# Kernel tuning notes

Hardware: AMD Instinct MI355X
Metric: run time of the kernel (lower is better)

Reference implementation:

```python
import jax, jax.numpy as jnp
import numpy as np


def _conv1x1(x, w, b):
    # x: [B,Cin,H,W], w: [Cout,Cin], b: [Cout]
    return jnp.einsum('bchw,oc->bohw', x, w) + b[None, :, None, None]


def setup_inputs() -> dict:
    key = jax.random.key(0)
    ks = jax.random.split(key, 9)
    C, Cb = 256, 128
    B, H, W = 8, 32, 32
    s_in = 1.0 / np.sqrt(C)
    s_bn = 1.0 / np.sqrt(Cb)
    return {
        'x': jax.random.normal(ks[0], (B, C, H, W), dtype=jnp.float32),
        'theta_w': jax.random.uniform(ks[1], (Cb, C), jnp.float32, -s_in, s_in),
        'theta_b': jax.random.uniform(ks[2], (Cb,), jnp.float32, -s_in, s_in),
        'phi_w': jax.random.uniform(ks[3], (Cb, C), jnp.float32, -s_in, s_in),
        'phi_b': jax.random.uniform(ks[4], (Cb,), jnp.float32, -s_in, s_in),
        'g_w': jax.random.uniform(ks[5], (Cb, C), jnp.float32, -s_in, s_in),
        'g_b': jax.random.uniform(ks[6], (Cb,), jnp.float32, -s_in, s_in),
        'W_w': jax.random.uniform(ks[7], (C, Cb), jnp.float32, -s_bn, s_bn),
        'W_b': jax.random.uniform(ks[8], (C,), jnp.float32, -s_bn, s_bn),
    }


def reference(x, theta_w, theta_b, phi_w, phi_b, g_w, g_b, W_w, W_b):
    B, C, H, Wd = x.shape
    Cb = theta_w.shape[0]
    theta = _conv1x1(x, theta_w, theta_b).reshape(-1, Cb)      # [N, Cb] (row-major, as torch)
    phi = _conv1x1(x, phi_w, phi_b).reshape(Cb, -1)            # [Cb, N]
    g = _conv1x1(x, g_w, g_b).reshape(-1, Cb)                  # [N, Cb]
    attn = jax.nn.softmax(theta @ phi, axis=1)                 # [N, N] global attention
    out = (attn @ g).reshape(B, -1, H, Wd)                     # [B, Cb, H, W]
    return _conv1x1(out, W_w, W_b) + x
```

## Files before the change

kernel.cpp:

```cpp
#include <hip/hip_runtime.h>

typedef unsigned short u16;
typedef __attribute__((ext_vector_type(8))) short short8;
typedef __attribute__((ext_vector_type(4))) float f32x4;

__device__ __forceinline__ u16 f2bf(float f){
  union { float f; unsigned u; } v; v.f = f;
  unsigned u = v.u;
  u += 0x7fffu + ((u >> 16) & 1u);
  return (u16)(u >> 16);
}
__device__ __forceinline__ float bf2f(u16 h){
  union { unsigned u; float f; } v; v.u = ((unsigned)h) << 16;
  return v.f;
}

__global__ __launch_bounds__(256) void xcast_kernel(
    const float* __restrict__ x, u16* __restrict__ XT)
{
  __shared__ float tile[64][69];
  const int b = blockIdx.z, c0 = blockIdx.y*64, hw0 = blockIdx.x*64;
  const int t = threadIdx.x;
  {
    int r = t >> 2, cs = (t & 3) * 16;
    const float* s = x + (size_t)(b*256 + c0 + r)*1024 + hw0 + cs;
    #pragma unroll
    for (int i=0;i<4;i++)
      *(float4*)&tile[r][cs + i*4] = *(const float4*)(s + i*4);
  }
  __syncthreads();
  {
    int hr = t >> 2, cc = (t & 3) * 16;
    __align__(16) u16 tmp[16];
    #pragma unroll
    for (int i=0;i<16;i++) tmp[i] = f2bf(tile[cc + i][hr]);
    u16* d = XT + (size_t)(b*1024 + hw0 + hr)*256 + c0 + cc;
    *(uint4*)d     = *(uint4*)&tmp[0];
    *(uint4*)(d+8) = *(uint4*)&tmp[8];
  }
}

__global__ __launch_bounds__(256, 2) void proj_mfma_kernel(
    const u16* __restrict__ XT,
    const float* __restrict__ tw, const float* __restrict__ pw,
    const float* __restrict__ gw,
    const float* __restrict__ tb, const float* __restrict__ pb,
    const float* __restrict__ gb,
    u16* __restrict__ T, u16* __restrict__ PHI, u16* __restrict__ G)
{
  __shared__ __align__(16) u16 Ws[128][136];
  __shared__ __align__(16) u16 Xs[128][136];
  const int proj = blockIdx.x, qg = blockIdx.y;
  const int b = qg >> 3, hw0 = (qg & 7) * 128;
  const int q0 = qg * 128;
  const float* Wf   = (proj==0) ? tw : (proj==1) ? pw : gw;
  const float* bias = (proj==0) ? tb : (proj==1) ? pb : gb;
  u16* out          = (proj==0) ? T  : (proj==1) ? PHI : G;
  const float scale = (proj==0) ? 1.4426950408889634f : 1.0f;
  const int t = threadIdx.x;
  const int wave = t >> 6, lane = t & 63;
  const int quad = lane >> 4, n16 = lane & 15;

  f32x4 acc[8][2];
  #pragma unroll
  for (int mt=0;mt<8;mt++)
    #pragma unroll
    for (int nt=0;nt<2;nt++){ f32x4 z = {0.f,0.f,0.f,0.f}; acc[mt][nt] = z; }

  for (int c0 = 0; c0 < 256; c0 += 128){
    __syncthreads();
    {
      int row = t >> 1, cb = (t & 1) * 64;
      const float* s1 = Wf + (size_t)row*256 + c0 + cb;
      #pragma unroll
      for (int i=0;i<16;i++){
        float4 v = *(const float4*)(s1 + i*4);
        u16* d = &Ws[row][cb + i*4];
        d[0]=f2bf(v.x); d[1]=f2bf(v.y); d[2]=f2bf(v.z); d[3]=f2bf(v.w);
      }
      const u16* s2 = XT + (size_t)(q0 + row)*256 + c0 + cb;
      #pragma unroll
      for (int i=0;i<8;i++)
        *(uint4*)&Xs[row][cb + i*8] = *(const uint4*)(s2 + i*8);
    }
    __syncthreads();
    #pragma unroll
    for (int kc=0; kc<4; kc++){
      short8 xf[2];
      #pragma unroll
      for (int nt=0;nt<2;nt++)
        xf[nt] = *(const short8*)&Xs[wave*32 + nt*16 + n16][kc*32 + quad*8];
      #pragma unroll
      for (int mt=0;mt<8;mt++){
        short8 wf = *(const short8*)&Ws[mt*16 + n16][kc*32 + quad*8];
        #pragma unroll
        for (int nt=0;nt<2;nt++)
          acc[mt][nt] = __builtin_amdgcn_mfma_f32_16x16x32_bf16(wf, xf[nt], acc[mt][nt], 0, 0, 0);
      }
    }
  }
  #pragma unroll
  for (int mt=0;mt<8;mt++){
    float4 bv = *(const float4*)&bias[mt*16 + quad*4];
    float bb[4] = {bv.x, bv.y, bv.z, bv.w};
    #pragma unroll
    for (int nt=0;nt<2;nt++)
      #pragma unroll
      for (int r=0;r<4;r++)
        out[(size_t)b*131072 + (size_t)(mt*16 + quad*4 + r)*1024
            + hw0 + wave*32 + nt*16 + n16] = f2bf((acc[mt][nt][r] + bb[r]) * scale);
  }
}

__global__ __launch_bounds__(256) void transpose_bf_kernel(
    const u16* __restrict__ src, u16* __restrict__ dst, int R, int C)
{
  __shared__ u16 tile[64][72];
  const int t = threadIdx.x;
  const int c0 = blockIdx.x*64, r0 = blockIdx.y*64;
  {
    int rr = t >> 2, cs = (t & 3) * 16;
    const u16* s = src + (size_t)(r0+rr)*C + c0 + cs;
    uint4 a0 = *(const uint4*)s;
    uint4 a1 = *(const uint4*)(s+8);
    *(uint4*)&tile[rr][cs]   = a0;
    *(uint4*)&tile[rr][cs+8] = a1;
  }
  __syncthreads();
  {
    int cc = t >> 2, rs = (t & 3) * 16;
    __align__(16) u16 tmp[16];
    #pragma unroll
    for (int i=0;i<16;i++) tmp[i] = tile[rs+i][cc];
    u16* d = dst + (size_t)(c0+cc)*R + r0 + rs;
    *(uint4*)d     = *(uint4*)&tmp[0];
    *(uint4*)(d+8) = *(uint4*)&tmp[8];
  }
}

__global__ __launch_bounds__(256, 2) void attn_kernel(
    const u16* __restrict__ Tq, const u16* __restrict__ Kk,
    const u16* __restrict__ Vt, u16* __restrict__ Opart,
    float* __restrict__ lpart)
{
  __shared__ __align__(16) u16 Ks[64][136];
  __shared__ __align__(16) u16 Vs[128][72];
  __shared__ __align__(16) u16 Pall[4][4608];

  const int t = threadIdx.x;
  const int wave = t >> 6, lane = t & 63;
  const int quad = lane >> 4, n16 = lane & 15;
  const int s  = blockIdx.x & 15;
  const int qg = blockIdx.x >> 4;
  const int q0 = qg*256 + wave*64;
  u16* Pw = Pall[wave];
  u16*   Os = Opart + (size_t)s * 1048576;
  float* ls = lpart + (size_t)s * 8192;

  short8 qa[4][4];
  #pragma unroll
  for (int mt=0;mt<4;mt++)
    #pragma unroll
    for (int kc=0;kc<4;kc++)
      qa[mt][kc] = *(const short8*)(Tq + (size_t)(q0 + mt*16 + n16)*128 + kc*32 + quad*8);

  f32x4 o[4][8];
  float lp[4];
  #pragma unroll
  for (int mt=0;mt<4;mt++){
    #pragma unroll
    for (int dt=0;dt<8;dt++){ f32x4 z = {0.f,0.f,0.f,0.f}; o[mt][dt] = z; }
    lp[mt] = 0.f;
  }

  const int krow = t >> 2, kcs = (t & 3) * 32;
  const int vrow = t >> 1, vcs = (t & 1) * 32;
  const int wmask = n16 & 14;

  for (int kt = s*8; kt < s*8 + 8; kt++){
    const int key0 = kt * 64;
    __syncthreads();
    #pragma unroll
    for (int i=0;i<4;i++)
      *(uint4*)&Ks[krow][kcs + i*8] =
        *(const uint4*)(Kk + (size_t)(key0 + krow)*128 + kcs + i*8);
    #pragma unroll
    for (int i=0;i<4;i++)
      *(uint4*)&Vs[vrow][vcs + i*8] =
        *(const uint4*)(Vt + (size_t)vrow*8192 + key0 + vcs + i*8);
    __syncthreads();

    #pragma unroll
    for (int ntk=0; ntk<4; ntk++){
      short8 kf[4];
      #pragma unroll
      for (int kc=0;kc<4;kc++)
        kf[kc] = *(const short8*)&Ks[ntk*16 + n16][kc*32 + quad*8];
      #pragma unroll
      for (int mtq=0;mtq<4;mtq++){
        f32x4 sa = {0.f,0.f,0.f,0.f};
        #pragma unroll
        for (int kc=0;kc<4;kc++)
          sa = __builtin_amdgcn_mfma_f32_16x16x32_bf16(kf[kc], qa[mtq][kc], sa, 0, 0, 0);
        u16 pb[4];
        #pragma unroll
        for (int r=0;r<4;r++){
          float pe = __builtin_amdgcn_exp2f(sa[r]);
          lp[mtq] += pe;
          pb[r] = f2bf(pe);
        }
        uint2 pk;
        pk.x = ((unsigned)pb[1] << 16) | pb[0];
        pk.y = ((unsigned)pb[3] << 16) | pb[2];
        *(uint2*)(Pw + (mtq*16 + n16)*72 + (((ntk*4 + quad) ^ wmask) << 2)) = pk;
      }
    }

    __builtin_amdgcn_s_waitcnt(0xC07F);

    #pragma unroll
    for (int kb=0; kb<2; kb++){
      short8 pf[4];
      #pragma unroll
      for (int mtq=0;mtq<4;mtq++)
        pf[mtq] = *(const short8*)(Pw + (mtq*16 + n16)*72 + (((kb*8 + quad*2) ^ wmask) << 2));
      __builtin_amdgcn_s_setprio(1);
      #pragma unroll
      for (int dt=0; dt<8; dt++){
        short8 vfd = *(const short8*)&Vs[dt*16 + n16][kb*32 + quad*8];
        #pragma unroll
        for (int mtq=0;mtq<4;mtq++)
          o[mtq][dt] = __builtin_amdgcn_mfma_f32_16x16x32_bf16(pf[mtq], vfd, o[mtq][dt], 0, 0, 0);
      }
      __builtin_amdgcn_s_setprio(0);
    }
  }

  float l[4];
  #pragma unroll
  for (int mt=0;mt<4;mt++){
    float v = lp[mt];
    v += __shfl_xor(v, 16, 64);
    v += __shfl_xor(v, 32, 64);
    l[mt] = v;
  }

  #pragma unroll
  for (int mt=0;mt<4;mt++){
    #pragma unroll
    for (int r=0;r<4;r++){
      __align__(16) u16 tmp[8];
      #pragma unroll
      for (int dt=0;dt<8;dt++) tmp[dt] = f2bf(o[mt][dt][r]);
      *(uint4*)(Os + (size_t)(q0 + mt*16 + quad*4 + r)*128 + n16*8) = *(uint4*)tmp;
    }
    if (lane < 16)
      ls[q0 + mt*16 + lane] = l[mt];
  }
}

__global__ __launch_bounds__(256) void merge_o_kernel(
    const u16* __restrict__ Opart, const float* __restrict__ lpart, int S,
    u16* __restrict__ OmT)
{
  __shared__ u16 Tm[32][136];
  __shared__ float lrow[32];
  const int t = threadIdx.x;
  const int row0 = blockIdx.x * 32;
  const int b  = row0 >> 10;
  const int j0 = (row0 >> 3) & 127;

  if (t < 32){
    float v = 0.f;
    for (int sp=0; sp<S; sp++) v += lpart[sp*8192 + row0 + t];
    lrow[t] = 1.0f / v;
  }

  const int rl = t >> 3;
  const int cb = (t & 7) * 16;
  float acc[16];
  #pragma unroll
  for (int j=0;j<16;j++) acc[j] = 0.f;
  for (int sp=0; sp<S; sp++){
    const u16* p = Opart + (size_t)sp*1048576 + (size_t)(row0 + rl)*128 + cb;
    #pragma unroll
    for (int q=0;q<2;q++){
      ushort4 v = *(const ushort4*)(p + q*8);
      ushort4 w = *(const ushort4*)(p + q*8 + 4);
      acc[q*8+0] += bf2f(v.x); acc[q*8+1] += bf2f(v.y);
      acc[q*8+2] += bf2f(v.z); acc[q*8+3] += bf2f(v.w);
      acc[q*8+4] += bf2f(w.x); acc[q*8+5] += bf2f(w.y);
      acc[q*8+6] += bf2f(w.z); acc[q*8+7] += bf2f(w.w);
    }
  }
  __syncthreads();
  const float inv = lrow[rl];
  #pragma unroll
  for (int j=0;j<16;j++){
    int cp = cb + j;
    int ch = (cp & 7)*16 + (cp >> 3);
    Tm[rl][ch] = f2bf(acc[j] * inv);
  }
  __syncthreads();
  {
    const int hwhi = t >> 5;
    const int chb  = (t & 31) * 4;
    #pragma unroll
    for (int c=0;c<4;c++){
      int ch = chb + c;
      __align__(8) u16 tmp[4];
      #pragma unroll
      for (int jl=0;jl<4;jl++) tmp[jl] = Tm[jl*8 + hwhi][ch];
      *(uint2*)(OmT + (size_t)(b*1024 + hwhi*128 + ch)*128 + j0) = *(uint2*)tmp;
    }
  }
}

__global__ __launch_bounds__(256, 2) void final_mfma_kernel(
    const float* __restrict__ Ww, const float* __restrict__ Wb,
    const u16* __restrict__ OmT, const float* __restrict__ x,
    float* __restrict__ outp)
{
  __shared__ __align__(16) u16 Ws[64][136];
  __shared__ __align__(16) u16 Os[128][136];
  const int co0 = blockIdx.x * 64, qg = blockIdx.y;
  const int b = qg >> 3, hw0 = (qg & 7) * 128;
  const int q0 = qg * 128;
  const int t = threadIdx.x;
  const int wave = t >> 6, lane = t & 63;
  const int quad = lane >> 4, n16 = lane & 15;

  {
    int row = t >> 2, cbf = (t & 3) * 32;
    const float* sw = Ww + (size_t)(co0 + row)*128 + cbf;
    #pragma unroll
    for (int i=0;i<8;i++){
      float4 v = *(const float4*)(sw + i*4);
      u16* d = &Ws[row][cbf + i*4];
      d[0]=f2bf(v.x); d[1]=f2bf(v.y); d[2]=f2bf(v.z); d[3]=f2bf(v.w);
    }
  }
  {
    int row = t >> 1, cb = (t & 1) * 64;
    const u16* so = OmT + (size_t)(q0 + row)*128 + cb;
    #pragma unroll
    for (int i=0;i<8;i++)
      *(uint4*)&Os[row][cb + i*8] = *(const uint4*)(so + i*8);
  }
  __syncthreads();

  f32x4 acc[4][2];
  #pragma unroll
  for (int mt=0;mt<4;mt++)
    #pragma unroll
    for (int nt=0;nt<2;nt++){ f32x4 z = {0.f,0.f,0.f,0.f}; acc[mt][nt] = z; }

  #pragma unroll
  for (int kc=0; kc<4; kc++){
    short8 xf[2];
    #pragma unroll
    for (int nt=0;nt<2;nt++)
      xf[nt] = *(const short8*)&Os[wave*32 + nt*16 + n16][kc*32 + quad*8];
    #pragma unroll
    for (int mt=0;mt<4;mt++){
      short8 wf = *(const short8*)&Ws[mt*16 + n16][kc*32 + quad*8];
      #pragma unroll
      for (int nt=0;nt<2;nt++)
        acc[mt][nt] = __builtin_amdgcn_mfma_f32_16x16x32_bf16(wf, xf[nt], acc[mt][nt], 0, 0, 0);
    }
  }

  #pragma unroll
  for (int mt=0;mt<4;mt++){
    float4 bv = *(const float4*)&Wb[co0 + mt*16 + quad*4];
    float bb[4] = {bv.x, bv.y, bv.z, bv.w};
    #pragma unroll
    for (int nt=0;nt<2;nt++)
      #pragma unroll
      for (int r=0;r<4;r++){
        size_t idx = (size_t)b*262144 + (size_t)(co0 + mt*16 + quad*4 + r)*1024
                   + hw0 + wave*32 + nt*16 + n16;
        outp[idx] = acc[mt][nt][r] + bb[r] + x[idx];
      }
  }
}

extern "C" void kernel_launch(void* const* d_in, const int* in_sizes, int n_in,
                              void* d_out, int out_size, void* d_ws, size_t ws_size,
                              hipStream_t stream)
{
  (void)in_sizes; (void)n_in; (void)out_size; (void)ws_size;
  const float* x  = (const float*)d_in[0];
  const float* tw = (const float*)d_in[1];
  const float* tb = (const float*)d_in[2];
  const float* pw = (const float*)d_in[3];
  const float* pb = (const float*)d_in[4];
  const float* gw = (const float*)d_in[5];
  const float* gb = (const float*)d_in[6];
  const float* Ww = (const float*)d_in[7];
  const float* Wb = (const float*)d_in[8];
  float* outp = (float*)d_out;

  char* ws = (char*)d_ws;
  const size_t MB = 1u << 20;
  u16*   Tbf   = (u16*)(ws);
  u16*   PHIbf = (u16*)(ws + 2*MB);
  u16*   Gbf   = (u16*)(ws + 4*MB);
  u16*   Kbf   = (u16*)(ws + 6*MB);
  u16*   VTbf  = (u16*)(ws + 8*MB);
  u16*   Opart = (u16*)(ws + 10*MB);
  u16*   XT    = (u16*)(ws + 10*MB);
  float* lpart = (float*)(ws + 2*MB);
  u16*   OmT   = (u16*)(ws + 4*MB);

  xcast_kernel<<<dim3(16, 4, 8), 256, 0, stream>>>(x, XT);
  proj_mfma_kernel<<<dim3(3, 64), 256, 0, stream>>>(XT, tw, pw, gw, tb, pb, gb,
                                                    Tbf, PHIbf, Gbf);
  transpose_bf_kernel<<<dim3(128, 2), 256, 0, stream>>>(PHIbf, Kbf, 128, 8192);
  transpose_bf_kernel<<<dim3(2, 128), 256, 0, stream>>>(Gbf, VTbf, 8192, 128);
  attn_kernel<<<dim3(512), 256, 0, stream>>>(Tbf, Kbf, VTbf, Opart, lpart);
  merge_o_kernel<<<dim3(256), 256, 0, stream>>>(Opart, lpart, 16, OmT);
  final_mfma_kernel<<<dim3(4, 64), 256, 0, stream>>>(Ww, Wb, OmT, x, outp);
}
```

Baseline: 162.9 us.

## Double-buffer K/V tiles via direct global-to-LDS loads in attention kernel

Restructures the attention kernel to use 512-thread blocks (8 waves, 512 queries per block) and double-buffered K/V shared tiles filled with global_load_lds, so the next key tile loads while the current one is computed. The LDS layout drops row padding in favour of an XOR swizzle to avoid bank conflicts. The goal is to hide global-load latency and halve the number of K/V loads per query. In exchange it uses more LDS, allows only one block per CU, and adds a full vmcnt wait plus a barrier every iteration.

```diff
diff --git a/kernel.cpp b/kernel.cpp
--- a/kernel.cpp
+++ b/kernel.cpp
@@ -13,6 +13,11 @@
 __device__ __forceinline__ float bf2f(u16 h){
   union { unsigned u; float f; } v; v.u = ((unsigned)h) << 16;
   return v.f;
+}
+__device__ __forceinline__ void gload16(const u16* g, u16* l){
+  __builtin_amdgcn_global_load_lds(
+      (const __attribute__((address_space(1))) unsigned int*)g,
+      (__attribute__((address_space(3))) unsigned int*)l, 16, 0, 0);
 }
 
 __global__ __launch_bounds__(256) void xcast_kernel(
@@ -138,21 +143,21 @@
   }
 }
 
-__global__ __launch_bounds__(256, 2) void attn_kernel(
+__global__ __launch_bounds__(512, 1) void attn_kernel(
     const u16* __restrict__ Tq, const u16* __restrict__ Kk,
     const u16* __restrict__ Vt, u16* __restrict__ Opart,
     float* __restrict__ lpart)
 {
-  __shared__ __align__(16) u16 Ks[64][136];
-  __shared__ __align__(16) u16 Vs[128][72];
-  __shared__ __align__(16) u16 Pall[4][4608];
+  __shared__ __align__(16) u16 Ks[2][8192];
+  __shared__ __align__(16) u16 Vs[2][8192];
+  __shared__ __align__(16) u16 Pall[8][4096];
 
   const int t = threadIdx.x;
   const int wave = t >> 6, lane = t & 63;
   const int quad = lane >> 4, n16 = lane & 15;
   const int s  = blockIdx.x & 15;
   const int qg = blockIdx.x >> 4;
-  const int q0 = qg*256 + wave*64;
+  const int q0 = qg*512 + wave*64;
   u16* Pw = Pall[wave];
   u16*   Os = Opart + (size_t)s * 1048576;
   float* ls = lpart + (size_t)s * 8192;
@@ -173,29 +178,46 @@
     lp[mt] = 0.f;
   }
 
-  const int krow = t >> 2, kcs = (t & 3) * 32;
-  const int vrow = t >> 1, vcs = (t & 1) * 32;
+  const int ck0   = wave * 2;
+  const int rk_l  = lane >> 4;
+  const int rv_l  = lane >> 3;
+  const int cbk_l = (lane & 15) * 16;
+  const int cbv_l = (lane & 7) * 16;
   const int wmask = n16 & 14;
-
-  for (int kt = s*8; kt < s*8 + 8; kt++){
-    const int key0 = kt * 64;
-    __syncthreads();
-    #pragma unroll
-    for (int i=0;i<4;i++)
-      *(uint4*)&Ks[krow][kcs + i*8] =
-        *(const uint4*)(Kk + (size_t)(key0 + krow)*128 + kcs + i*8);
-    #pragma unroll
-    for (int i=0;i<4;i++)
-      *(uint4*)&Vs[vrow][vcs + i*8] =
-        *(const uint4*)(Vt + (size_t)vrow*8192 + key0 + vcs + i*8);
-    __syncthreads();
+  const int swz   = (n16 & 7) << 4;
+
+  auto STAGE = [&](int bi, int key0){
+    #pragma unroll
+    for (int i=0;i<2;i++){
+      const int ck = ck0 + i;
+      const int rk = ck*4 + rk_l;
+      gload16(Kk + (size_t)(key0 + rk)*128 + ((cbk_l ^ ((rk & 7) << 4)) >> 1),
+              &Ks[bi][ck*512]);
+    }
+    #pragma unroll
+    for (int i=0;i<2;i++){
+      const int ck = ck0 + i;
+      const int rv = ck*8 + rv_l;
+      gload16(Vt + (size_t)rv*8192 + key0 + ((cbv_l ^ ((rv & 7) << 4)) >> 1),
+              &Vs[bi][ck*512]);
+    }
+  };
+
+  STAGE(0, s*512);
+  asm volatile("s_waitcnt vmcnt(0)" ::: "memory");
+  __syncthreads();
+
+  int bi = 0;
+  for (int kt = 0; kt < 8; kt++){
+    if (kt < 7) STAGE(bi^1, (s*8 + kt + 1)*64);
 
     #pragma unroll
     for (int ntk=0; ntk<4; ntk++){
       short8 kf[4];
       #pragma unroll
       for (int kc=0;kc<4;kc++)
-        kf[kc] = *(const short8*)&Ks[ntk*16 + n16][kc*32 + quad*8];
+        kf[kc] = *(const short8*)((const char*)&Ks[bi][0]
+                   + ((ntk*16 + n16) << 8) + ((kc*64 + quad*16) ^ swz));
       #pragma unroll
       for (int mtq=0;mtq<4;mtq++){
         f32x4 sa = {0.f,0.f,0.f,0.f};
@@ -212,7 +234,7 @@
         uint2 pk;
         pk.x = ((unsigned)pb[1] << 16) | pb[0];
         pk.y = ((unsigned)pb[3] << 16) | pb[2];
-        *(uint2*)(Pw + (mtq*16 + n16)*72 + (((ntk*4 + quad) ^ wmask) << 2)) = pk;
+        *(uint2*)(Pw + (mtq*16 + n16)*64 + (((ntk*4 + quad) ^ wmask) << 2)) = pk;
       }
     }
 
@@ -223,16 +245,23 @@
       short8 pf[4];
       #pragma unroll
       for (int mtq=0;mtq<4;mtq++)
-        pf[mtq] = *(const short8*)(Pw + (mtq*16 + n16)*72 + (((kb*8 + quad*2) ^ wmask) << 2));
+        pf[mtq] = *(const short8*)(Pw + (mtq*16 + n16)*64 + (((kb*8 + quad*2) ^ wmask) << 2));
       __builtin_amdgcn_s_setprio(1);
       #pragma unroll
       for (int dt=0; dt<8; dt++){
-        short8 vfd = *(const short8*)&Vs[dt*16 + n16][kb*32 + quad*8];
+        short8 vfd = *(const short8*)((const char*)&Vs[bi][0]
+                       + ((dt*16 + n16) << 7) + ((kb*64 + quad*16) ^ swz));
         #pragma unroll
         for (int mtq=0;mtq<4;mtq++)
           o[mtq][dt] = __builtin_amdgcn_mfma_f32_16x16x32_bf16(pf[mtq], vfd, o[mtq][dt], 0, 0, 0);
       }
       __builtin_amdgcn_s_setprio(0);
+    }
+
+    if (kt < 7){
+      asm volatile("s_waitcnt vmcnt(0)" ::: "memory");
+      __syncthreads();
+      bi ^= 1;
     }
   }
 
@@ -418,7 +447,7 @@
                                                     Tbf, PHIbf, Gbf);
   transpose_bf_kernel<<<dim3(128, 2), 256, 0, stream>>>(PHIbf, Kbf, 128, 8192);
   transpose_bf_kernel<<<dim3(2, 128), 256, 0, stream>>>(Gbf, VTbf, 8192, 128);
-  attn_kernel<<<dim3(512), 256, 0, stream>>>(Tbf, Kbf, VTbf, Opart, lpart);
+  attn_kernel<<<dim3(256), 512, 0, stream>>>(Tbf, Kbf, VTbf, Opart, lpart);
   merge_o_kernel<<<dim3(256), 256, 0, stream>>>(Opart, lpart, 16, OmT);
   final_mfma_kernel<<<dim3(4, 64), 256, 0, stream>>>(Ww, Wb, OmT, x, outp);
 }
```

Result: slower. 223.6 us (+37.2%).

## Split attention block into producer and consumer waves with register-prefetched K/V tiles

Applied to the files above, without the earlier changes.

The attention kernel now launches 512 threads per block. The upper four waves act as producers: they prefetch the next K and V tile into registers while the lower four waves run the QK^T, exp and PV MFMA work on the current tile. The goal is to hide global-load latency behind compute instead of making the compute waves do their own loads between barriers. The cost is doubled block size, with register limits set by launch_bounds(512,2) that may cause spills in the consumers holding large accumulators, and producer waves that sit idle during compute.

```diff
diff --git a/kernel.cpp b/kernel.cpp
--- a/kernel.cpp
+++ b/kernel.cpp
@@ -138,7 +138,7 @@
   }
 }
 
-__global__ __launch_bounds__(256, 2) void attn_kernel(
+__global__ __launch_bounds__(512, 2) void attn_kernel(
     const u16* __restrict__ Tq, const u16* __restrict__ Kk,
     const u16* __restrict__ Vt, u16* __restrict__ Opart,
     float* __restrict__ lpart)
@@ -150,112 +150,135 @@
   const int t = threadIdx.x;
   const int wave = t >> 6, lane = t & 63;
   const int quad = lane >> 4, n16 = lane & 15;
+  const bool producer = (t >= 256);
   const int s  = blockIdx.x & 15;
   const int qg = blockIdx.x >> 4;
-  const int q0 = qg*256 + wave*64;
-  u16* Pw = Pall[wave];
+  const int q0 = qg*256 + (wave & 3)*64;
+  u16* Pw = Pall[wave & 3];
   u16*   Os = Opart + (size_t)s * 1048576;
   float* ls = lpart + (size_t)s * 8192;
 
+  const int pt   = t & 255;
+  const int krow = pt >> 2, kcs = (pt & 3) * 32;
+  const int vrow = pt >> 1, vcs = (pt & 1) * 32;
+  const int wmask = n16 & 14;
+
   short8 qa[4][4];
-  #pragma unroll
-  for (int mt=0;mt<4;mt++)
-    #pragma unroll
-    for (int kc=0;kc<4;kc++)
-      qa[mt][kc] = *(const short8*)(Tq + (size_t)(q0 + mt*16 + n16)*128 + kc*32 + quad*8);
-
   f32x4 o[4][8];
   float lp[4];
-  #pragma unroll
-  for (int mt=0;mt<4;mt++){
-    #pragma unroll
-    for (int dt=0;dt<8;dt++){ f32x4 z = {0.f,0.f,0.f,0.f}; o[mt][dt] = z; }
-    lp[mt] = 0.f;
-  }
-
-  const int krow = t >> 2, kcs = (t & 3) * 32;
-  const int vrow = t >> 1, vcs = (t & 1) * 32;
-  const int wmask = n16 & 14;
-
-  for (int kt = s*8; kt < s*8 + 8; kt++){
-    const int key0 = kt * 64;
+  uint4 kr[4], vr[4];
+
+  if (producer){
+    const int key0 = s*512;
+    #pragma unroll
+    for (int i=0;i<4;i++)
+      kr[i] = *(const uint4*)(Kk + (size_t)(key0 + krow)*128 + kcs + i*8);
+    #pragma unroll
+    for (int i=0;i<4;i++)
+      vr[i] = *(const uint4*)(Vt + (size_t)vrow*8192 + key0 + vcs + i*8);
+  } else {
+    #pragma unroll
+    for (int mt=0;mt<4;mt++)
+      #pragma unroll
+      for (int kc=0;kc<4;kc++)
+        qa[mt][kc] = *(const short8*)(Tq + (size_t)(q0 + mt*16 + n16)*128 + kc*32 + quad*8);
+    #pragma unroll
+    for (int mt=0;mt<4;mt++){
+      #pragma unroll
+      for (int dt=0;dt<8;dt++){ f32x4 z = {0.f,0.f,0.f,0.f}; o[mt][dt] = z; }
+      lp[mt] = 0.f;
+    }
+  }
+
+  for (int kt = 0; kt < 8; kt++){
     __syncthreads();
-    #pragma unroll
-    for (int i=0;i<4;i++)
-      *(uint4*)&Ks[krow][kcs + i*8] =
-        *(const uint4*)(Kk + (size_t)(key0 + krow)*128 + kcs + i*8);
-    #pragma unroll
-    for (int i=0;i<4;i++)
-      *(uint4*)&Vs[vrow][vcs + i*8] =
-        *(const uint4*)(Vt + (size_t)vrow*8192 + key0 + vcs + i*8);
+    if (producer){
+      #pragma unroll
+      for (int i=0;i<4;i++) *(uint4*)&Ks[krow][kcs + i*8] = kr[i];
+      #pragma unroll
+      for (int i=0;i<4;i++) *(uint4*)&Vs[vrow][vcs + i*8] = vr[i];
+    }
     __syncthreads();
-
-    #pragma unroll
-    for (int ntk=0; ntk<4; ntk++){
-      short8 kf[4];
-      #pragma unroll
-      for (int kc=0;kc<4;kc++)
-        kf[kc] = *(const short8*)&Ks[ntk*16 + n16][kc*32 + quad*8];
-      #pragma unroll
-      for (int mtq=0;mtq<4;mtq++){
-        f32x4 sa = {0.f,0.f,0.f,0.f};
+    if (producer){
+      if (kt < 7){
+        const int key0 = (s*8 + kt + 1)*64;
+        #pragma unroll
+        for (int i=0;i<4;i++)
+          kr[i] = *(const uint4*)(Kk + (size_t)(key0 + krow)*128 + kcs + i*8);
+        #pragma unroll
+        for (int i=0;i<4;i++)
+          vr[i] = *(const uint4*)(Vt + (size_t)vrow*8192 + key0 + vcs + i*8);
+      }
+    } else {
+      #pragma unroll
+      for (int ntk=0; ntk<4; ntk++){
+        short8 kf[4];
         #pragma unroll
         for (int kc=0;kc<4;kc++)
-          sa = __builtin_amdgcn_mfma_f32_16x16x32_bf16(kf[kc], qa[mtq][kc], sa, 0, 0, 0);
-        u16 pb[4];
-        #pragma unroll
-        for (int r=0;r<4;r++){
-          float pe = __builtin_amdgcn_exp2f(sa[r]);
-          lp[mtq] += pe;
-          pb[r] = f2bf(pe);
+          kf[kc] = *(const short8*)&Ks[ntk*16 + n16][kc*32 + quad*8];
+        #pragma unroll
+        for (int mtq=0;mtq<4;mtq++){
+          f32x4 sa = {0.f,0.f,0.f,0.f};
+          #pragma unroll
+          for (int kc=0;kc<4;kc++)
+            sa = __builtin_amdgcn_mfma_f32_16x16x32_bf16(kf[kc], qa[mtq][kc], sa, 0, 0, 0);
+          u16 pb[4];
+          #pragma unroll
+          for (int r=0;r<4;r++){
+            float pe = __builtin_amdgcn_exp2f(sa[r]);
+            lp[mtq] += pe;
+            pb[r] = f2bf(pe);
+          }
+          uint2 pk;
+          pk.x = ((unsigned)pb[1] << 16) | pb[0];
+          pk.y = ((unsigned)pb[3] << 16) | pb[2];
+          *(uint2*)(Pw + (mtq*16 + n16)*72 + (((ntk*4 + quad) ^ wmask) << 2)) = pk;
         }
-        uint2 pk;
-        pk.x = ((unsigned)pb[1] << 16) | pb[0];
-        pk.y = ((unsigned)pb[3] << 16) | pb[2];
-        *(uint2*)(Pw + (mtq*16 + n16)*72 + (((ntk*4 + quad) ^ wmask) << 2)) = pk;
-      }
-    }
-
-    __builtin_amdgcn_s_waitcnt(0xC07F);
-
-    #pragma unroll
-    for (int kb=0; kb<2; kb++){
-      short8 pf[4];
-      #pragma unroll
-      for (int mtq=0;mtq<4;mtq++)
-        pf[mtq] = *(const short8*)(Pw + (mtq*16 + n16)*72 + (((kb*8 + quad*2) ^ wmask) << 2));
-      __builtin_amdgcn_s_setprio(1);
-      #pragma unroll
-      for (int dt=0; dt<8; dt++){
-        short8 vfd = *(const short8*)&Vs[dt*16 + n16][kb*32 + quad*8];
+      }
+
+      __builtin_amdgcn_s_waitcnt(0xC07F);
+
+      #pragma unroll
+      for (int kb=0; kb<2; kb++){
+        short8 pf[4];
         #pragma unroll
         for (int mtq=0;mtq<4;mtq++)
-          o[mtq][dt] = __builtin_amdgcn_mfma_f32_16x16x32_bf16(pf[mtq], vfd, o[mtq][dt], 0, 0, 0);
-      }
-      __builtin_amdgcn_s_setprio(0);
-    }
-  }
-
-  float l[4];
-  #pragma unroll
-  for (int mt=0;mt<4;mt++){
-    float v = lp[mt];
-    v += __shfl_xor(v, 16, 64);
-    v += __shfl_xor(v, 32, 64);
-    l[mt] = v;
-  }
-
-  #pragma unroll
-  for (int mt=0;mt<4;mt++){
-    #pragma unroll
-    for (int r=0;r<4;r++){
-      __align__(16) u16 tmp[8];
-      #pragma unroll
-      for (int dt=0;dt<8;dt++) tmp[dt] = f2bf(o[mt][dt][r]);
-      *(uint4*)(Os + (size_t)(q0 + mt*16 + quad*4 + r)*128 + n16*8) = *(uint4*)tmp;
-    }
-    if (lane < 16)
-      ls[q0 + mt*16 + lane] = l[mt];
+          pf[mtq] = *(const short8*)(Pw + (mtq*16 + n16)*72 + (((kb*8 + quad*2) ^ wmask) << 2));
+        __builtin_amdgcn_s_setprio(1);
+        #pragma unroll
+        for (int dt=0; dt<8; dt++){
+          short8 vfd = *(const short8*)&Vs[dt*16 + n16][kb*32 + quad*8];
+          #pragma unroll
+          for (int mtq=0;mtq<4;mtq++)
+            o[mtq][dt] = __builtin_amdgcn_mfma_f32_16x16x32_bf16(pf[mtq], vfd, o[mtq][dt], 0, 0, 0);
+        }
+        __builtin_amdgcn_s_setprio(0);
+      }
+    }
+  }
+
+  if (!producer){
+    float l[4];
+    #pragma unroll
+    for (int mt=0;mt<4;mt++){
+      float v = lp[mt];
+      v += __shfl_xor(v, 16, 64);
+      v += __shfl_xor(v, 32, 64);
+      l[mt] = v;
+    }
+
+    #pragma unroll
+    for (int mt=0;mt<4;mt++){
+      #pragma unroll
+      for (int r=0;r<4;r++){
+        __align__(16) u16 tmp[8];
+        #pragma unroll
+        for (int dt=0;dt<8;dt++) tmp[dt] = f2bf(o[mt][dt][r]);
+        *(uint4*)(Os + (size_t)(q0 + mt*16 + quad*4 + r)*128 + n16*8) = *(uint4*)tmp;
+      }
+      if (lane < 16)
+        ls[q0 + mt*16 + lane] = l[mt];
+    }
   }
 }
 
@@ -418,7 +441,7 @@
                                                     Tbf, PHIbf, Gbf);
   transpose_bf_kernel<<<dim3(128, 2), 256, 0, stream>>>(PHIbf, Kbf, 128, 8192);
   transpose_bf_kernel<<<dim3(2, 128), 256, 0, stream>>>(Gbf, VTbf, 8192, 128);
-  attn_kernel<<<dim3(512), 256, 0, stream>>>(Tbf, Kbf, VTbf, Opart, lpart);
+  attn_kernel<<<dim3(512), 512, 0, stream>>>(Tbf, Kbf, VTbf, Opart, lpart);
   merge_o_kernel<<<dim3(256), 256, 0, stream>>>(Opart, lpart, 16, OmT);
   final_mfma_kernel<<<dim3(4, 64), 256, 0, stream>>>(Ww, Wb, OmT, x, outp);
 }
```

Result: slower. 212.1 us (+30.2%).

## Keep softmax probabilities in registers and feed PV via 16x16x16 bf16 MFMA

Applied to the files above, without the earlier changes.

Removes the per-wave shared-memory staging of the exponentiated score tile, which was written and re-read between the QK and PV matmuls. The QK accumulator layout is reused directly as the A operand of a K=16 bf16 MFMA, so P never leaves registers. In exchange PV uses the older 16x16x16 MFMA, which takes twice as many instructions, and it reads narrower V fragments from shared memory. The change also drops 36KB of LDS use, which may allow higher occupancy.

```diff
diff --git a/kernel.cpp b/kernel.cpp
--- a/kernel.cpp
+++ b/kernel.cpp
@@ -2,7 +2,14 @@
 
 typedef unsigned short u16;
 typedef __attribute__((ext_vector_type(8))) short short8;
+typedef __attribute__((ext_vector_type(4))) short short4v;
 typedef __attribute__((ext_vector_type(4))) float f32x4;
+
+#if __has_builtin(__builtin_amdgcn_mfma_f32_16x16x16bf16_1k)
+#define PV16 1
+#else
+#define PV16 0
+#endif
 
 __device__ __forceinline__ u16 f2bf(float f){
   union { float f; unsigned u; } v; v.f = f;
@@ -145,7 +152,9 @@
 {
   __shared__ __align__(16) u16 Ks[64][136];
   __shared__ __align__(16) u16 Vs[128][72];
+#if !PV16
   __shared__ __align__(16) u16 Pall[4][4608];
+#endif
 
   const int t = threadIdx.x;
   const int wave = t >> 6, lane = t & 63;
@@ -153,7 +162,10 @@
   const int s  = blockIdx.x & 15;
   const int qg = blockIdx.x >> 4;
   const int q0 = qg*256 + wave*64;
+#if !PV16
   u16* Pw = Pall[wave];
+  const int wmask = n16 & 14;
+#endif
   u16*   Os = Opart + (size_t)s * 1048576;
   float* ls = lpart + (size_t)s * 8192;
 
@@ -175,7 +187,6 @@
 
   const int krow = t >> 2, kcs = (t & 3) * 32;
   const int vrow = t >> 1, vcs = (t & 1) * 32;
-  const int wmask = n16 & 14;
 
   for (int kt = s*8; kt < s*8 + 8; kt++){
     const int key0 = kt * 64;
@@ -190,6 +201,43 @@
         *(const uint4*)(Vt + (size_t)vrow*8192 + key0 + vcs + i*8);
     __syncthreads();
 
+#if PV16
+    #pragma unroll
+    for (int ntk=0; ntk<4; ntk++){
+      short8 kf[4];
+      #pragma unroll
+      for (int kc=0;kc<4;kc++)
+        kf[kc] = *(const short8*)&Ks[ntk*16 + n16][kc*32 + quad*8];
+      short4v pa[4];
+      #pragma unroll
+      for (int mtq=0;mtq<4;mtq++){
+        f32x4 sa = {0.f,0.f,0.f,0.f};
+        #pragma unroll
+        for (int kc=0;kc<4;kc++)
+          sa = __builtin_amdgcn_mfma_f32_16x16x32_bf16(kf[kc], qa[mtq][kc], sa, 0, 0, 0);
+        u16 pb[4];
+        #pragma unroll
+        for (int r=0;r<4;r++){
+          float pe = __builtin_amdgcn_exp2f(sa[r]);
+          lp[mtq] += pe;
+          pb[r] = f2bf(pe);
+        }
+        union { unsigned u[2]; short4v v; } pu;
+        pu.u[0] = ((unsigned)pb[1] << 16) | pb[0];
+        pu.u[1] = ((unsigned)pb[3] << 16) | pb[2];
+        pa[mtq] = pu.v;
+      }
+      __builtin_amdgcn_s_setprio(1);
+      #pragma unroll
+      for (int dt=0; dt<8; dt++){
+        short4v vb = *(const short4v*)&Vs[dt*16 + n16][ntk*16 + quad*4];
+        #pragma unroll
+        for (int mtq=0;mtq<4;mtq++)
+          o[mtq][dt] = __builtin_amdgcn_mfma_f32_16x16x16bf16_1k(pa[mtq], vb, o[mtq][dt], 0, 0, 0);
+      }
+      __builtin_amdgcn_s_setprio(0);
+    }
+#else
     #pragma unroll
     for (int ntk=0; ntk<4; ntk++){
       short8 kf[4];
@@ -215,9 +263,7 @@
         *(uint2*)(Pw + (mtq*16 + n16)*72 + (((ntk*4 + quad) ^ wmask) << 2)) = pk;
       }
     }
-
     __builtin_amdgcn_s_waitcnt(0xC07F);
-
     #pragma unroll
     for (int kb=0; kb<2; kb++){
       short8 pf[4];
@@ -234,6 +280,7 @@
       }
       __builtin_amdgcn_s_setprio(0);
     }
+#endif
   }
 
   float l[4];
```

New measurement: 221.1 us. +35.7%, slower.
